# Kernel optimization log

Measured on AMD Instinct MI355X. Metric: run time of the kernel, lower is better.

The kernel has to match this reference:

```python
import jax, jax.numpy as jnp
import numpy as np

BS, T, HS, WS = 2, 4, 32, 32
HW = HS * WS
D, NH, NL, NP = 256, 8, 4, 4
HD = D // NH
DFFN = 1024


def layer_norm(x, g, b, eps=1e-5):
    mu = jnp.mean(x, axis=-1, keepdims=True)
    var = jnp.mean((x - mu) ** 2, axis=-1, keepdims=True)
    return (x - mu) * jax.lax.rsqrt(var + eps) * g + b


def bilinear_gather(val, loc, Hl, Wl):
    # val: (bs, nh, Hl*Wl, hd); loc: (bs, Lq, nh, P, 2) in [0,1], last dim (x, y)
    # matches F.grid_sample(align_corners=False, padding_mode='zeros') on grid=2*loc-1
    x = loc[..., 0] * Wl - 0.5
    y = loc[..., 1] * Hl - 0.5
    x0 = jnp.floor(x)
    y0 = jnp.floor(y)
    lx = x - x0
    ly = y - y0
    bs, Lq, nh, P = x.shape
    out = jnp.zeros((bs, nh, Lq * P, val.shape[-1]), val.dtype)
    for dy in (0, 1):
        for dx in (0, 1):
            xi = x0 + dx
            yi = y0 + dy
            w = (lx if dx else 1.0 - lx) * (ly if dy else 1.0 - ly)
            valid = (xi >= 0) & (xi < Wl) & (yi >= 0) & (yi < Hl)
            w = jnp.where(valid, w, 0.0)
            xi_c = jnp.clip(xi, 0, Wl - 1).astype(jnp.int32)
            yi_c = jnp.clip(yi, 0, Hl - 1).astype(jnp.int32)
            idx = (yi_c * Wl + xi_c).transpose(0, 2, 1, 3).reshape(bs, nh, Lq * P)
            g = jnp.take_along_axis(val, idx[..., None], axis=2)
            wt = w.transpose(0, 2, 1, 3).reshape(bs, nh, Lq * P)
            out = out + wt[..., None] * g
    return out.reshape(bs, nh, Lq, P, val.shape[-1])


def setup_inputs() -> dict:
    key = jax.random.key(0)
    ks = jax.random.split(key, 12)
    s = 0.02
    return {
        "src": jax.random.normal(ks[0], (BS, T, HW, D), jnp.float32),
        "pos": jax.random.normal(ks[1], (BS, T, HW, D), jnp.float32),
        "reference_points": jax.random.uniform(ks[2], (BS, T * HW, NL, 2), jnp.float32),
        "value_proj_w": jax.random.normal(ks[3], (D, D), jnp.float32) * s,
        "value_proj_b": jnp.zeros((D,), jnp.float32),
        "sampling_offsets_w": jax.random.normal(ks[4], (D, NH * NL * NP * 2), jnp.float32) * s,
        "sampling_offsets_b": jax.random.normal(ks[5], (NH * NL * NP * 2,), jnp.float32) * s,
        "attn_weights_w": jax.random.normal(ks[6], (D, NH * NL * NP), jnp.float32) * s,
        "attn_weights_b": jnp.zeros((NH * NL * NP,), jnp.float32),
        "output_proj_w": jax.random.normal(ks[7], (D, D), jnp.float32) * s,
        "output_proj_b": jnp.zeros((D,), jnp.float32),
        "norm1_g": jnp.ones((D,), jnp.float32),
        "norm1_b": jnp.zeros((D,), jnp.float32),
        "linear1_w": jax.random.normal(ks[8], (D, DFFN), jnp.float32) * s,
        "linear1_b": jnp.zeros((DFFN,), jnp.float32),
        "linear2_w": jax.random.normal(ks[9], (DFFN, D), jnp.float32) * s,
        "linear2_b": jnp.zeros((D,), jnp.float32),
        "norm2_g": jnp.ones((D,), jnp.float32),
        "norm2_b": jnp.zeros((D,), jnp.float32),
        "spatial_shapes": np.array([[HS, WS]] * NL, np.int32),
        "level_start_index": np.arange(NL, dtype=np.int32) * HW,
    }


def reference(src, pos, reference_points, value_proj_w, value_proj_b,
              sampling_offsets_w, sampling_offsets_b, attn_weights_w, attn_weights_b,
              output_proj_w, output_proj_b, norm1_g, norm1_b,
              linear1_w, linear1_b, linear2_w, linear2_b, norm2_g, norm2_b,
              spatial_shapes, level_start_index):
    bs, t, hw, d = src.shape
    Lq = t * hw
    x = src.reshape(bs, Lq, d)
    q = x  # module never adds pos in forward (with_pos_embed unused)
    value = (x @ value_proj_w + value_proj_b).reshape(bs, Lq, NH, HD)
    offsets = (q @ sampling_offsets_w + sampling_offsets_b).reshape(bs, Lq, NH, NL, NP, 2)
    aw = jax.nn.softmax((q @ attn_weights_w + attn_weights_b).reshape(bs, Lq, NH, NL * NP), axis=-1)
    aw = aw.reshape(bs, Lq, NH, NL, NP)
    ss = np.asarray(spatial_shapes)
    lsi = np.asarray(level_start_index)
    offset_normalizer = jnp.asarray(ss[:, ::-1].copy(), src.dtype)  # (L, 2) = (W, H)
    sampling_locations = reference_points[:, :, None, :, None, :] + offsets / offset_normalizer[None, None, None, :, None, :]
    attn_out = jnp.zeros((bs, NH, Lq, HD), src.dtype)
    for l in range(NL):
        Hl, Wl = int(ss[l, 0]), int(ss[l, 1])
        start = int(lsi[l])
        v_l = value[:, start:start + Hl * Wl].transpose(0, 2, 1, 3)  # (bs, nh, HlWl, hd)
        samp = bilinear_gather(v_l, sampling_locations[:, :, :, l], Hl, Wl)  # (bs, nh, Lq, P, hd)
        w_l = aw[:, :, :, l].transpose(0, 2, 1, 3)  # (bs, nh, Lq, P)
        attn_out = attn_out + jnp.sum(samp * w_l[..., None], axis=3)
    attn_out = attn_out.transpose(0, 2, 1, 3).reshape(bs, Lq, d) @ output_proj_w + output_proj_b
    x = layer_norm(x + attn_out, norm1_g, norm1_b)
    ffn = jax.nn.relu(x @ linear1_w + linear1_b) @ linear2_w + linear2_b
    x = layer_norm(x + ffn, norm2_g, norm2_b)
    return x.reshape(bs, t, hw, d), sampling_locations
```

## Files before the change

### kernel.cpp

```cpp
#include <hip/hip_runtime.h>
#include <math.h>

#define ROWS   8192
#define LQ     4096
#define NHEAD  8
#define NLVL   4
#define NPTS   4
#define HDIM   32

typedef __attribute__((ext_vector_type(8))) short v8s;
typedef __attribute__((ext_vector_type(4))) float v4f;

__device__ __forceinline__ unsigned short f2bf(float x) {
    unsigned int u = __float_as_uint(x);
    u += 0x7fffu + ((u >> 16) & 1u);
    return (unsigned short)(u >> 16);
}
__device__ __forceinline__ float bf2f(unsigned short x) {
    return __uint_as_float(((unsigned int)x) << 16);
}

__device__ __forceinline__ void glds16(const void* g, void* l) {
    __builtin_amdgcn_global_load_lds(
        (const __attribute__((address_space(1))) unsigned int*)g,
        (__attribute__((address_space(3))) unsigned int*)l, 16, 0, 0);
}

__device__ __forceinline__ void trans_tile(const float* __restrict__ in,
                                           unsigned short* __restrict__ out,
                                           int K, int N, int ldout, int n_off,
                                           int bx, int by, int tid)
{
    __shared__ float t[32][33];
    int tx = tid & 31, ty = tid >> 5;
    int k0 = by << 5, n0 = bx << 5;
    #pragma unroll
    for (int i = 0; i < 4; i++)
        t[ty + i * 8][tx] = in[(size_t)(k0 + ty + i * 8) * N + n0 + tx];
    __syncthreads();
    #pragma unroll
    for (int i = 0; i < 4; i++)
        out[(size_t)(n_off + n0 + ty + i * 8) * ldout + k0 + tx] = f2bf(t[tx][ty + i * 8]);
}

__global__ __launch_bounds__(256) void prep_k(
    const float* __restrict__ src, unsigned short* __restrict__ src_bf,
    const float* __restrict__ vw, const float* __restrict__ ofw,
    const float* __restrict__ aww, const float* __restrict__ pw,
    const float* __restrict__ w1, const float* __restrict__ w2,
    unsigned short* __restrict__ Btcat, unsigned short* __restrict__ pwT,
    unsigned short* __restrict__ w1T, unsigned short* __restrict__ w2T,
    const float* __restrict__ vb, const float* __restrict__ ofb,
    const float* __restrict__ awb, float* __restrict__ biascat)
{
    int bid = blockIdx.x, tid = threadIdx.x;
    if (bid < 2048) {
        int i = bid * 256 + tid;
        float4 v = ((const float4*)src)[i];
        ushort4 o;
        o.x = f2bf(v.x); o.y = f2bf(v.y); o.z = f2bf(v.z); o.w = f2bf(v.w);
        ((ushort4*)src_bf)[i] = o;
    } else if (bid < 2112) {
        int t = bid - 2048; trans_tile(vw, Btcat, 256, 256, 256, 0, t & 7, t >> 3, tid);
    } else if (bid < 2176) {
        int t = bid - 2112; trans_tile(ofw, Btcat, 256, 256, 256, 256, t & 7, t >> 3, tid);
    } else if (bid < 2208) {
        int t = bid - 2176; trans_tile(aww, Btcat, 256, 128, 256, 512, t & 3, t >> 2, tid);
    } else if (bid < 2272) {
        int t = bid - 2208; trans_tile(pw, pwT, 256, 256, 256, 0, t & 7, t >> 3, tid);
    } else if (bid < 2528) {
        int t = bid - 2272; trans_tile(w1, w1T, 256, 1024, 256, 0, t & 31, t >> 5, tid);
    } else if (bid < 2784) {
        int t = bid - 2528; trans_tile(w2, w2T, 1024, 256, 1024, 0, t & 7, t >> 3, tid);
    } else {
        biascat[tid] = vb[tid];
        biascat[tid + 256] = ofb[tid];
        if (tid < 128) biascat[tid + 512] = awb[tid];
    }
}

template<bool PROJ, bool OUTBF, bool RELU, bool RES>
__global__ __launch_bounds__(256) void mfma_gemm_k(
    const unsigned short* __restrict__ A,
    const unsigned short* __restrict__ Bt,
    const float* __restrict__ bias,
    const float* __restrict__ res,
    void* __restrict__ Cout,
    unsigned short* __restrict__ vbf,
    const float* __restrict__ refp,
    float* __restrict__ oloc,
    int M, int N, int K)
{
    __shared__ __align__(16) unsigned short As[4096];
    __shared__ __align__(16) unsigned short Bs[2048];
    const int tid = threadIdx.x;
    const int row0 = blockIdx.y << 7, col0 = blockIdx.x << 6;
    const int wid = tid >> 6, lane = tid & 63;
    const int wm = wid & 1, wn = wid >> 1;
    const int lr = lane & 15, kq = lane >> 4;

    v4f acc[4][2];
    #pragma unroll
    for (int i = 0; i < 4; i++)
        #pragma unroll
        for (int j = 0; j < 2; j++) acc[i][j] = (v4f){0.f, 0.f, 0.f, 0.f};

    for (int k0 = 0; k0 < K; k0 += 32) {
        __syncthreads();
        #pragma unroll
        for (int i = 0; i < 2; i++) {
            int c = wid * 128 + i * 64 + lane;
            int row = c >> 2;
            int kk = ((c & 3) + (row >> 2)) & 3;
            glds16(A + (size_t)(row0 + row) * K + k0 + kk * 8,
                   &As[(wid * 128 + i * 64) * 8]);
        }
        {
            int c = wid * 64 + lane;
            int row = c >> 2;
            int kk = ((c & 3) + (row >> 2)) & 3;
            glds16(Bt + (size_t)(col0 + row) * K + k0 + kk * 8,
                   &Bs[wid * 512]);
        }
        __syncthreads();
        v8s bf[2];
        #pragma unroll
        for (int nt = 0; nt < 2; nt++) {
            int row = wn * 32 + nt * 16 + lr;
            int s = (kq - (row >> 2)) & 3;
            bf[nt] = *(const v8s*)(&Bs[(row * 4 + s) * 8]);
        }
        #pragma unroll
        for (int mt = 0; mt < 4; mt++) {
            int row = wm * 64 + mt * 16 + lr;
            int s = (kq - (row >> 2)) & 3;
            v8s af = *(const v8s*)(&As[(row * 4 + s) * 8]);
            #pragma unroll
            for (int nt = 0; nt < 2; nt++)
                acc[mt][nt] = __builtin_amdgcn_mfma_f32_16x16x32_bf16(af, bf[nt], acc[mt][nt], 0, 0, 0);
        }
    }

    const int rq = lane >> 4;
    #pragma unroll
    for (int mt = 0; mt < 4; mt++) {
        #pragma unroll
        for (int nt = 0; nt < 2; nt++) {
            int col = col0 + wn * 32 + nt * 16 + lr;
            float bv = bias[col];
            #pragma unroll
            for (int i = 0; i < 4; i++) {
                int row = row0 + wm * 64 + mt * 16 + rq * 4 + i;
                float v = acc[mt][nt][i] + bv;
                if (RELU) v = fmaxf(v, 0.f);
                if (RES)  v += res[(size_t)row * N + col];
                if (PROJ) {
                    if (col0 < 256) {
                        int b = row >> 12, rb = row & 4095;
                        int l = rb >> 10, pix = rb & 1023;
                        int h = col >> 5, d = col & 31;
                        size_t idx = ((size_t)(((b << 2) + l) * 8 + h) << 15) + (pix << 5) + d;
                        vbf[idx] = f2bf(v);
                    } else if (col0 < 512) {
                        int colm = col - 256;
                        int l = (colm >> 3) & 3, cc = colm & 1;
                        oloc[(size_t)row * 256 + colm] =
                            refp[(size_t)row * 8 + l * 2 + cc] + v * (1.f / 32.f);
                    } else {
                        ((float*)Cout)[(size_t)row * 128 + col - 512] = v;
                    }
                } else if (OUTBF) {
                    ((unsigned short*)Cout)[(size_t)row * N + col] = f2bf(v);
                } else {
                    ((float*)Cout)[(size_t)row * N + col] = v;
                }
            }
        }
    }
}

template<bool OUTBF, bool RELU, bool RES>
__global__ __launch_bounds__(256) void mfma_gemm64_k(
    const unsigned short* __restrict__ A,
    const unsigned short* __restrict__ Bt,
    const float* __restrict__ bias,
    const float* __restrict__ res,
    void* __restrict__ Cout,
    int M, int N, int K)
{
    __shared__ __align__(16) unsigned short As[2048];
    __shared__ __align__(16) unsigned short Bs[2048];
    const int tid = threadIdx.x;
    const int row0 = blockIdx.y << 6, col0 = blockIdx.x << 6;
    const int wid = tid >> 6, lane = tid & 63;
    const int lr = lane & 15, kq = lane >> 4;

    v4f acc[4];
    #pragma unroll
    for (int i = 0; i < 4; i++) acc[i] = (v4f){0.f, 0.f, 0.f, 0.f};

    for (int k0 = 0; k0 < K; k0 += 32) {
        __syncthreads();
        {
            int c = wid * 64 + lane;
            int row = c >> 2;
            int kk = ((c & 3) + (row >> 2)) & 3;
            glds16(A + (size_t)(row0 + row) * K + k0 + kk * 8, &As[wid * 512]);
            glds16(Bt + (size_t)(col0 + row) * K + k0 + kk * 8, &Bs[wid * 512]);
        }
        __syncthreads();
        int colr = wid * 16 + lr;
        int sb = (kq - (colr >> 2)) & 3;
        v8s bf = *(const v8s*)(&Bs[(colr * 4 + sb) * 8]);
        #pragma unroll
        for (int mt = 0; mt < 4; mt++) {
            int rowr = mt * 16 + lr;
            int sa = (kq - (rowr >> 2)) & 3;
            v8s af = *(const v8s*)(&As[(rowr * 4 + sa) * 8]);
            acc[mt] = __builtin_amdgcn_mfma_f32_16x16x32_bf16(af, bf, acc[mt], 0, 0, 0);
        }
    }

    const int rq = lane >> 4;
    const int col = col0 + wid * 16 + lr;
    float bv = bias[col];
    #pragma unroll
    for (int mt = 0; mt < 4; mt++) {
        #pragma unroll
        for (int i = 0; i < 4; i++) {
            int row = row0 + mt * 16 + rq * 4 + i;
            float v = acc[mt][i] + bv;
            if (RELU) v = fmaxf(v, 0.f);
            if (RES)  v += res[(size_t)row * N + col];
            if (OUTBF) ((unsigned short*)Cout)[(size_t)row * N + col] = f2bf(v);
            else       ((float*)Cout)[(size_t)row * N + col] = v;
        }
    }
}

__global__ __launch_bounds__(256) void gather_lds_k(
    const float* __restrict__ po,
    const unsigned short* __restrict__ vbf,
    const float* __restrict__ loc,
    float* __restrict__ part)
{
    int bid = blockIdx.x, tid = threadIdx.x;
    int h = bid & 7, rc = (bid >> 3) & 7, l = (bid >> 6) & 3, b = bid >> 8;

    __shared__ __align__(16) unsigned short vt[32768];

    const unsigned short* vsub = vbf + (((size_t)(((b << 2) + l) * 8 + h)) << 15);
    int wv = tid >> 6, lane = tid & 63;
    #pragma unroll
    for (int i = 0; i < 16; i++) {
        int base = i * 256 + wv * 64;
        glds16(vsub + (size_t)(base + lane) * 8, &vt[base * 8]);
    }
    __syncthreads();

    int g = tid >> 3, d4 = tid & 7;
    int rbase = b * 4096 + rc * 512;
    #pragma unroll 2
    for (int i = 0; i < 16; i++) {
        int r = rbase + g + i * 32;
        float2 lg = *(const float2*)(po + (size_t)r * 128 + h * 16 + d4 * 2);
        float m = fmaxf(lg.x, lg.y);
        m = fmaxf(m, __shfl_xor(m, 1, 8));
        m = fmaxf(m, __shfl_xor(m, 2, 8));
        m = fmaxf(m, __shfl_xor(m, 4, 8));
        float e0 = __expf(lg.x - m), e1 = __expf(lg.y - m);
        float s = e0 + e1;
        s += __shfl_xor(s, 1, 8);
        s += __shfl_xor(s, 2, 8);
        s += __shfl_xor(s, 4, 8);
        float inv = 1.f / s;
        float ww0 = e0 * inv, ww1 = e1 * inv;
        float wgt[4];
        wgt[0] = __shfl(ww0, l * 2, 8);
        wgt[1] = __shfl(ww1, l * 2, 8);
        wgt[2] = __shfl(ww0, l * 2 + 1, 8);
        wgt[3] = __shfl(ww1, l * 2 + 1, 8);

        float locv[8];
        *(float4*)(locv)     = *(const float4*)(loc + (size_t)r * 256 + h * 32 + l * 8);
        *(float4*)(locv + 4) = *(const float4*)(loc + (size_t)r * 256 + h * 32 + l * 8 + 4);

        float a0 = 0.f, a1 = 0.f, a2 = 0.f, a3 = 0.f;
        #pragma unroll
        for (int p = 0; p < 4; p++) {
            float xf = locv[p * 2] * 32.f - 0.5f, yf = locv[p * 2 + 1] * 32.f - 0.5f;
            float x0f = floorf(xf), y0f = floorf(yf);
            float fx = xf - x0f, fy = yf - y0f;
            int x0 = (int)x0f, y0 = (int)y0f;
            #pragma unroll
            for (int dy = 0; dy < 2; dy++) {
                #pragma unroll
                for (int dx = 0; dx < 2; dx++) {
                    int xi = x0 + dx, yi = y0 + dy;
                    float wt = (dx ? fx : 1.f - fx) * (dy ? fy : 1.f - fy);
                    bool valid = (xi >= 0) & (xi < 32) & (yi >= 0) & (yi < 32);
                    int xc = min(max(xi, 0), 31), yc = min(max(yi, 0), 31);
                    float c = valid ? (wgt[p] * wt) : 0.f;
                    ushort4 u = *(const ushort4*)(&vt[((yc << 5) + xc) * 32 + d4 * 4]);
                    a0 += c * bf2f(u.x); a1 += c * bf2f(u.y);
                    a2 += c * bf2f(u.z); a3 += c * bf2f(u.w);
                }
            }
        }
        float4 o = {a0, a1, a2, a3};
        *(float4*)(part + (size_t)l * 2097152 + (size_t)r * 256 + h * 32 + d4 * 4) = o;
    }
}

__global__ __launch_bounds__(256) void reduce_k(
    const float* __restrict__ part, unsigned short* __restrict__ attn_bf)
{
    int i = blockIdx.x * 256 + threadIdx.x;
    const float4* p = (const float4*)part;
    float4 a = p[i];
    float4 b = p[i + 524288];
    float4 c = p[i + 1048576];
    float4 d = p[i + 1572864];
    ushort4 o;
    o.x = f2bf(a.x + b.x + c.x + d.x);
    o.y = f2bf(a.y + b.y + c.y + d.y);
    o.z = f2bf(a.z + b.z + c.z + d.z);
    o.w = f2bf(a.w + b.w + c.w + d.w);
    ((ushort4*)attn_bf)[i] = o;
}

template<bool WRITE_BF>
__global__ __launch_bounds__(256) void layernorm_k(
    float* __restrict__ x, const float* __restrict__ g, const float* __restrict__ b,
    unsigned short* __restrict__ xbf)
{
    int lane = threadIdx.x & 63;
    int wv = threadIdx.x >> 6;
    int row = blockIdx.x * 4 + wv;
    int c = lane << 2;
    float4 v = *(const float4*)(x + (size_t)row * 256 + c);
    float s = v.x + v.y + v.z + v.w;
    #pragma unroll
    for (int o = 1; o < 64; o <<= 1) s += __shfl_xor(s, o);
    float mu = s * (1.f / 256.f);
    float d0 = v.x - mu, d1 = v.y - mu, d2 = v.z - mu, d3 = v.w - mu;
    float vs = d0 * d0 + d1 * d1 + d2 * d2 + d3 * d3;
    #pragma unroll
    for (int o = 1; o < 64; o <<= 1) vs += __shfl_xor(vs, o);
    float rstd = rsqrtf(vs * (1.f / 256.f) + 1e-5f);
    float4 gg = *(const float4*)(g + c);
    float4 bb = *(const float4*)(b + c);
    float4 o4;
    o4.x = d0 * rstd * gg.x + bb.x;
    o4.y = d1 * rstd * gg.y + bb.y;
    o4.z = d2 * rstd * gg.z + bb.z;
    o4.w = d3 * rstd * gg.w + bb.w;
    *(float4*)(x + (size_t)row * 256 + c) = o4;
    if (WRITE_BF) {
        ushort4 ob;
        ob.x = f2bf(o4.x); ob.y = f2bf(o4.y); ob.z = f2bf(o4.z); ob.w = f2bf(o4.w);
        *(ushort4*)(xbf + (size_t)row * 256 + c) = ob;
    }
}

extern "C" void kernel_launch(void* const* d_in, const int* in_sizes, int n_in,
                              void* d_out, int out_size, void* d_ws, size_t ws_size,
                              hipStream_t stream)
{
    const float* src   = (const float*)d_in[0];
    const float* refp  = (const float*)d_in[2];
    const float* vw    = (const float*)d_in[3];
    const float* vb    = (const float*)d_in[4];
    const float* ofw   = (const float*)d_in[5];
    const float* ofb   = (const float*)d_in[6];
    const float* aww   = (const float*)d_in[7];
    const float* awb   = (const float*)d_in[8];
    const float* pw    = (const float*)d_in[9];
    const float* pb    = (const float*)d_in[10];
    const float* g1    = (const float*)d_in[11];
    const float* b1    = (const float*)d_in[12];
    const float* w1    = (const float*)d_in[13];
    const float* bi1   = (const float*)d_in[14];
    const float* w2    = (const float*)d_in[15];
    const float* bi2   = (const float*)d_in[16];
    const float* g2    = (const float*)d_in[17];
    const float* b2    = (const float*)d_in[18];

    float* ws = (float*)d_ws;
    float*          po        = ws;
    float*          x1        = ws + 1048576;
    unsigned short* value_bf  = (unsigned short*)(ws + 3145728);
    unsigned short* src_bf    = (unsigned short*)(ws + 4194304);
    unsigned short* x1_bf     = (unsigned short*)(ws + 5242880);
    unsigned short* attn_bf   = (unsigned short*)(ws + 6291456);
    unsigned short* hidden_bf = (unsigned short*)(ws + 7340032);
    unsigned short* Btcat     = (unsigned short*)(ws + 11534336);
    unsigned short* pwT       = (unsigned short*)(ws + 11616256);
    unsigned short* w1T       = (unsigned short*)(ws + 11649024);
    unsigned short* w2T       = (unsigned short*)(ws + 11780096);
    float*          biascat   = ws + 11911168;
    float*          part      = ws + 11912192;

    float* out_x   = (float*)d_out;
    float* out_loc = out_x + 2097152;

    dim3 blk(256);

    prep_k<<<2785, blk, 0, stream>>>(src, src_bf, vw, ofw, aww, pw, w1, w2,
                                     Btcat, pwT, w1T, w2T, vb, ofb, awb, biascat);

    mfma_gemm_k<true, false, false, false><<<dim3(10, 64), blk, 0, stream>>>(
        src_bf, Btcat, biascat, nullptr, po, value_bf, refp, out_loc, ROWS, 640, 256);

    gather_lds_k<<<512, blk, 0, stream>>>(po, value_bf, out_loc, part);
    reduce_k<<<2048, blk, 0, stream>>>(part, attn_bf);

    mfma_gemm64_k<false, false, true><<<dim3(4, 128), blk, 0, stream>>>(
        attn_bf, pwT, pb, src, x1, ROWS, 256, 256);
    layernorm_k<true><<<2048, blk, 0, stream>>>(x1, g1, b1, x1_bf);

    mfma_gemm_k<false, true, true, false><<<dim3(16, 64), blk, 0, stream>>>(
        x1_bf, w1T, bi1, nullptr, hidden_bf, nullptr, nullptr, nullptr, ROWS, 1024, 256);
    mfma_gemm64_k<false, false, true><<<dim3(4, 128), blk, 0, stream>>>(
        hidden_bf, w2T, bi2, x1, out_x, ROWS, 256, 1024);
    layernorm_k<false><<<2048, blk, 0, stream>>>(out_x, g2, b2, nullptr);
}
```

Baseline: 196.9 us.

## Fuse level reduction into gather kernel with double-buffered LDS value tiles

The gather kernel now loops over all four levels inside one block, accumulating in registers, and writes bf16 attention output directly. Value tiles for the next level are prefetched into a second LDS buffer while the current level is processed. This removes the fp32 per-level partial buffer and the separate reduce kernel, at the cost of fewer blocks, double LDS usage and reduced occupancy.

Result: slower. 212.8 us (+8.1%).

```diff
diff --git a/kernel.cpp b/kernel.cpp
--- a/kernel.cpp
+++ b/kernel.cpp
@@ -242,91 +242,98 @@
     const float* __restrict__ po,
     const unsigned short* __restrict__ vbf,
     const float* __restrict__ loc,
-    float* __restrict__ part)
+    unsigned short* __restrict__ attn_bf)
 {
     int bid = blockIdx.x, tid = threadIdx.x;
-    int h = bid & 7, rc = (bid >> 3) & 7, l = (bid >> 6) & 3, b = bid >> 8;
-
-    __shared__ __align__(16) unsigned short vt[32768];
-
-    const unsigned short* vsub = vbf + (((size_t)(((b << 2) + l) * 8 + h)) << 15);
-    int wv = tid >> 6, lane = tid & 63;
+    int h = bid & 7, rc = (bid >> 3) & 15, b = bid >> 7;
+
+    __shared__ __align__(16) unsigned short vt[2][32768];
+
+    const int wv = tid >> 6, lane = tid & 63;
+    const unsigned short* vbase_bh = vbf + (((size_t)(b * 4 * 8 + h)) << 15);
+
     #pragma unroll
     for (int i = 0; i < 16; i++) {
         int base = i * 256 + wv * 64;
-        glds16(vsub + (size_t)(base + lane) * 8, &vt[base * 8]);
-    }
-    __syncthreads();
-
-    int g = tid >> 3, d4 = tid & 7;
-    int rbase = b * 4096 + rc * 512;
-    #pragma unroll 2
-    for (int i = 0; i < 16; i++) {
-        int r = rbase + g + i * 32;
-        float2 lg = *(const float2*)(po + (size_t)r * 128 + h * 16 + d4 * 2);
-        float m = fmaxf(lg.x, lg.y);
-        m = fmaxf(m, __shfl_xor(m, 1, 8));
-        m = fmaxf(m, __shfl_xor(m, 2, 8));
-        m = fmaxf(m, __shfl_xor(m, 4, 8));
-        float e0 = __expf(lg.x - m), e1 = __expf(lg.y - m);
-        float s = e0 + e1;
-        s += __shfl_xor(s, 1, 8);
-        s += __shfl_xor(s, 2, 8);
-        s += __shfl_xor(s, 4, 8);
-        float inv = 1.f / s;
-        float ww0 = e0 * inv, ww1 = e1 * inv;
-        float wgt[4];
-        wgt[0] = __shfl(ww0, l * 2, 8);
-        wgt[1] = __shfl(ww1, l * 2, 8);
-        wgt[2] = __shfl(ww0, l * 2 + 1, 8);
-        wgt[3] = __shfl(ww1, l * 2 + 1, 8);
-
-        float locv[8];
-        *(float4*)(locv)     = *(const float4*)(loc + (size_t)r * 256 + h * 32 + l * 8);
-        *(float4*)(locv + 4) = *(const float4*)(loc + (size_t)r * 256 + h * 32 + l * 8 + 4);
-
-        float a0 = 0.f, a1 = 0.f, a2 = 0.f, a3 = 0.f;
-        #pragma unroll
-        for (int p = 0; p < 4; p++) {
-            float xf = locv[p * 2] * 32.f - 0.5f, yf = locv[p * 2 + 1] * 32.f - 0.5f;
-            float x0f = floorf(xf), y0f = floorf(yf);
-            float fx = xf - x0f, fy = yf - y0f;
-            int x0 = (int)x0f, y0 = (int)y0f;
+        glds16(vbase_bh + (size_t)(base + lane) * 8, &vt[0][base * 8]);
+    }
+
+    const int g = tid >> 3, d4 = tid & 7;
+    const int rbase = b * 4096 + rc * 256;
+
+    float4 acc8[8];
+    #pragma unroll
+    for (int i = 0; i < 8; i++) acc8[i] = (float4){0.f, 0.f, 0.f, 0.f};
+
+    for (int l = 0; l < 4; l++) {
+        __syncthreads();
+        if (l < 3) {
+            const unsigned short* vnext =
+                vbase_bh + (((size_t)((l + 1) * 8)) << 15);
             #pragma unroll
-            for (int dy = 0; dy < 2; dy++) {
+            for (int i = 0; i < 16; i++) {
+                int base = i * 256 + wv * 64;
+                glds16(vnext + (size_t)(base + lane) * 8, &vt[(l + 1) & 1][base * 8]);
+            }
+        }
+        const unsigned short* vtl = &vt[l & 1][0];
+
+        #pragma unroll 2
+        for (int i = 0; i < 8; i++) {
+            int r = rbase + g + i * 32;
+            float2 lg = *(const float2*)(po + (size_t)r * 128 + h * 16 + d4 * 2);
+            float m = fmaxf(lg.x, lg.y);
+            m = fmaxf(m, __shfl_xor(m, 1, 8));
+            m = fmaxf(m, __shfl_xor(m, 2, 8));
+            m = fmaxf(m, __shfl_xor(m, 4, 8));
+            float e0 = __expf(lg.x - m), e1 = __expf(lg.y - m);
+            float s = e0 + e1;
+            s += __shfl_xor(s, 1, 8);
+            s += __shfl_xor(s, 2, 8);
+            s += __shfl_xor(s, 4, 8);
+            float inv = 1.f / s;
+            float ww0 = e0 * inv, ww1 = e1 * inv;
+            float wgt[4];
+            wgt[0] = __shfl(ww0, l * 2, 8);
+            wgt[1] = __shfl(ww1, l * 2, 8);
+            wgt[2] = __shfl(ww0, l * 2 + 1, 8);
+            wgt[3] = __shfl(ww1, l * 2 + 1, 8);
+
+            float locv[8];
+            *(float4*)(locv)     = *(const float4*)(loc + (size_t)r * 256 + h * 32 + l * 8);
+            *(float4*)(locv + 4) = *(const float4*)(loc + (size_t)r * 256 + h * 32 + l * 8 + 4);
+
+            #pragma unroll
+            for (int p = 0; p < 4; p++) {
+                float xf = locv[p * 2] * 32.f - 0.5f, yf = locv[p * 2 + 1] * 32.f - 0.5f;
+                float x0f = floorf(xf), y0f = floorf(yf);
+                float fx = xf - x0f, fy = yf - y0f;
+                int x0 = (int)x0f, y0 = (int)y0f;
                 #pragma unroll
-                for (int dx = 0; dx < 2; dx++) {
-                    int xi = x0 + dx, yi = y0 + dy;
-                    float wt = (dx ? fx : 1.f - fx) * (dy ? fy : 1.f - fy);
-                    bool valid = (xi >= 0) & (xi < 32) & (yi >= 0) & (yi < 32);
-                    int xc = min(max(xi, 0), 31), yc = min(max(yi, 0), 31);
-                    float c = valid ? (wgt[p] * wt) : 0.f;
-                    ushort4 u = *(const ushort4*)(&vt[((yc << 5) + xc) * 32 + d4 * 4]);
-                    a0 += c * bf2f(u.x); a1 += c * bf2f(u.y);
-                    a2 += c * bf2f(u.z); a3 += c * bf2f(u.w);
+                for (int dy = 0; dy < 2; dy++) {
+                    #pragma unroll
+                    for (int dx = 0; dx < 2; dx++) {
+                        int xi = x0 + dx, yi = y0 + dy;
+                        float wt = (dx ? fx : 1.f - fx) * (dy ? fy : 1.f - fy);
+                        bool valid = (xi >= 0) & (xi < 32) & (yi >= 0) & (yi < 32);
+                        int xc = min(max(xi, 0), 31), yc = min(max(yi, 0), 31);
+                        float c = valid ? (wgt[p] * wt) : 0.f;
+                        ushort4 u = *(const ushort4*)(&vtl[((yc << 5) + xc) * 32 + d4 * 4]);
+                        acc8[i].x += c * bf2f(u.x); acc8[i].y += c * bf2f(u.y);
+                        acc8[i].z += c * bf2f(u.z); acc8[i].w += c * bf2f(u.w);
+                    }
                 }
             }
         }
-        float4 o = {a0, a1, a2, a3};
-        *(float4*)(part + (size_t)l * 2097152 + (size_t)r * 256 + h * 32 + d4 * 4) = o;
-    }
-}
-
-__global__ __launch_bounds__(256) void reduce_k(
-    const float* __restrict__ part, unsigned short* __restrict__ attn_bf)
-{
-    int i = blockIdx.x * 256 + threadIdx.x;
-    const float4* p = (const float4*)part;
-    float4 a = p[i];
-    float4 b = p[i + 524288];
-    float4 c = p[i + 1048576];
-    float4 d = p[i + 1572864];
-    ushort4 o;
-    o.x = f2bf(a.x + b.x + c.x + d.x);
-    o.y = f2bf(a.y + b.y + c.y + d.y);
-    o.z = f2bf(a.z + b.z + c.z + d.z);
-    o.w = f2bf(a.w + b.w + c.w + d.w);
-    ((ushort4*)attn_bf)[i] = o;
+    }
+    #pragma unroll
+    for (int i = 0; i < 8; i++) {
+        int r = rbase + g + i * 32;
+        ushort4 o;
+        o.x = f2bf(acc8[i].x); o.y = f2bf(acc8[i].y);
+        o.z = f2bf(acc8[i].z); o.w = f2bf(acc8[i].w);
+        *(ushort4*)(attn_bf + (size_t)r * 256 + h * 32 + d4 * 4) = o;
+    }
 }
 
 template<bool WRITE_BF>
@@ -399,7 +406,6 @@
     unsigned short* w1T       = (unsigned short*)(ws + 11649024);
     unsigned short* w2T       = (unsigned short*)(ws + 11780096);
     float*          biascat   = ws + 11911168;
-    float*          part      = ws + 11912192;
 
     float* out_x   = (float*)d_out;
     float* out_loc = out_x + 2097152;
@@ -412,8 +418,7 @@
     mfma_gemm_k<true, false, false, false><<<dim3(10, 64), blk, 0, stream>>>(
         src_bf, Btcat, biascat, nullptr, po, value_bf, refp, out_loc, ROWS, 640, 256);
 
-    gather_lds_k<<<512, blk, 0, stream>>>(po, value_bf, out_loc, part);
-    reduce_k<<<2048, blk, 0, stream>>>(part, attn_bf);
+    gather_lds_k<<<256, blk, 0, stream>>>(po, value_bf, out_loc, attn_bf);
 
     mfma_gemm64_k<false, false, true><<<dim3(4, 128), blk, 0, stream>>>(
         attn_bf, pwT, pb, src, x1, ROWS, 256, 256);
```
